# Kernel optimization log

Hardware: AMD Instinct MI355X
Metric: run time of the kernel (lower is better)

Reference implementation:

```python
import jax, jax.numpy as jnp
import numpy as np

B, L, D, DIN, S, R, K = 2, 1024, 1024, 2048, 16, 64, 4


def setup_inputs() -> dict:
    key = jax.random.key(0)
    ks = jax.random.split(key, 8)
    f = lambda k, sh, sc: jax.random.normal(k, sh, jnp.float32) * sc
    return {
        "x": f(ks[0], (B, L, D), 1.0),
        "norm_w": jnp.ones((D,), jnp.float32),
        "W_in": f(ks[1], (D, 2 * DIN), D ** -0.5),
        "conv_w": f(ks[2], (DIN, 1, K), 0.5),
        "conv_b": jnp.zeros((DIN,), jnp.float32),
        "W_x": f(ks[3], (DIN, R + 2 * S), DIN ** -0.5),
        "W_dt": f(ks[4], (R, DIN), R ** -0.5),
        "b_dt": f(ks[5], (DIN,), 0.1),
        "A_log": jnp.log(jnp.broadcast_to(jnp.arange(1, S + 1, dtype=jnp.float32), (DIN, S))),
        "D_skip": jnp.ones((DIN,), jnp.float32),
        "W_out": f(ks[6], (DIN, D), DIN ** -0.5),
    }


def reference(x, norm_w, W_in, conv_w, conv_b, W_x, W_dt, b_dt, A_log, D_skip, W_out):
    eps = 1e-5
    # RMSNorm
    xn = x * jax.lax.rsqrt(jnp.mean(x * x, axis=-1, keepdims=True) + eps) * norm_w
    # input projection -> (x_branch, gate)
    xz = xn @ W_in                       # [B,L,2*DIN]
    xi, z = jnp.split(xz, 2, axis=-1)
    # causal depthwise conv1d along L
    xt = jnp.transpose(xi, (0, 2, 1))    # [B,DIN,L]
    xc = jax.lax.conv_general_dilated(xt, conv_w, (1,), [(K - 1, 0)],
                                      feature_group_count=DIN)
    xc = jnp.transpose(xc, (0, 2, 1)) + conv_b
    xc = jax.nn.silu(xc)                 # [B,L,DIN]
    # input-dependent SSM parameters
    xd = xc @ W_x                        # [B,L,R+2S]
    dt, Bm, Cm = jnp.split(xd, [R, R + S], axis=-1)
    dt = jax.nn.softplus(dt @ W_dt + b_dt)           # [B,L,DIN]
    A = -jnp.exp(A_log)                              # [DIN,S]
    dA = jnp.exp(dt[..., None] * A)                  # [B,L,DIN,S]
    dBu = (dt * xc)[..., None] * Bm[:, :, None, :]   # [B,L,DIN,S]
    # selective scan: h_t = dA_t * h_{t-1} + dBu_t (parallel associative scan)
    def comb(c1, c2):
        a1, b1 = c1
        a2, b2 = c2
        return a1 * a2, a2 * b1 + b2
    _, h = jax.lax.associative_scan(comb, (dA, dBu), axis=1)
    y = jnp.einsum('blds,bls->bld', h, Cm) + D_skip * xc
    y = y * jax.nn.silu(z)
    return x + y @ W_out
```

## Files before the change

kernel.cpp:

```cpp
#include <hip/hip_runtime.h>

#define B_    2
#define L_    1024
#define D_    1024
#define DIN_  2048
#define S_    16
#define R_    64
#define NTOK  (B_ * L_)
#define NCH   32
#define LC    (L_ / NCH)

typedef unsigned short u16;
typedef short bf16x8 __attribute__((ext_vector_type(8)));
typedef float f32x4  __attribute__((ext_vector_type(4)));

__device__ __forceinline__ u16 f2bf(float f) {
    union { float f; unsigned u; } v; v.f = f;
    return (u16)((v.u + 0x7FFFu + ((v.u >> 16) & 1u)) >> 16);
}

__global__ __launch_bounds__(256) void rmsnorm_kernel(
    const float* __restrict__ x, const float* __restrict__ w, u16* __restrict__ xn) {
    int row = blockIdx.x;
    const float4 v = ((const float4*)(x + (size_t)row * D_))[threadIdx.x];
    float ss = v.x * v.x + v.y * v.y + v.z * v.z + v.w * v.w;
#pragma unroll
    for (int o = 32; o > 0; o >>= 1) ss += __shfl_down(ss, o);
    __shared__ float red[4];
    if ((threadIdx.x & 63) == 0) red[threadIdx.x >> 6] = ss;
    __syncthreads();
    float tot = red[0] + red[1] + red[2] + red[3];
    float sc = rsqrtf(tot * (1.f / (float)D_) + 1e-5f);
    const float4 wv = ((const float4*)w)[threadIdx.x];
    ushort4 o;
    o.x = f2bf(v.x * sc * wv.x);
    o.y = f2bf(v.y * sc * wv.y);
    o.z = f2bf(v.z * sc * wv.z);
    o.w = f2bf(v.w * sc * wv.w);
    ((ushort4*)(xn + (size_t)row * D_))[threadIdx.x] = o;
}

__global__ __launch_bounds__(256) void transpose_f32_to_bf16(
    const float* __restrict__ src, u16* __restrict__ dst, int R, int Csrc) {
    __shared__ float tile[32][33];
    int c0 = blockIdx.x * 32, r0 = blockIdx.y * 32;
    int tx = threadIdx.x & 31, ty = threadIdx.x >> 5;
#pragma unroll
    for (int i = 0; i < 32; i += 8)
        tile[ty + i][tx] = (c0 + tx < Csrc)
            ? src[(size_t)(r0 + ty + i) * Csrc + c0 + tx] : 0.f;
    __syncthreads();
#pragma unroll
    for (int i = 0; i < 32; i += 8)
        dst[(size_t)(c0 + ty + i) * R + r0 + tx] = f2bf(tile[tx][ty + i]);
}

#define BK 32
template<int BM, int BN>
__global__ __launch_bounds__(256) void gemm_bf16(
    const u16* __restrict__ A, int lda,
    const u16* __restrict__ Bt, int ldb,
    float* __restrict__ C, u16* __restrict__ Cbf, int ldc,
    const float* __restrict__ aux,
    int M, int N, int K, int mode) {
    constexpr int WGM = (BM >= 128) ? 2 : 1;
    constexpr int WGN = 4 / WGM;
    constexpr int FM = BM / (16 * WGM);
    constexpr int FN = BN / (16 * WGN);
    constexpr int ABYTES = BM * BK * 2;
    constexpr int BBYTES = BN * BK * 2;
    __shared__ __align__(16) u16 As[2][BM * BK];
    __shared__ __align__(16) u16 Bs[2][BN * BK];
    const int t = threadIdx.x;
    const int w = t >> 6;
    const int l = t & 63;
    const int lr = l & 15;
    const int kg = l >> 4;
    const int wm = (w / WGN) * (BM / WGM);
    const int wn = (w % WGN) * (BN / WGN);

    int nwg = gridDim.x * gridDim.y * gridDim.z;
    int flat = blockIdx.x + gridDim.x * (blockIdx.y + gridDim.y * blockIdx.z);
    int swz = (flat & 7) * (nwg >> 3) + (flat >> 3);
    int bx = swz % gridDim.x;
    int rem = swz / gridDim.x;
    int by = rem % gridDim.y;
    int bz = rem / gridDim.y;

    const int row0 = by * BM;
    const int col0 = bx * BN;
    const int kbase = bz * K;

    auto stage = [&](int buf, int k0) {
#pragma unroll
        for (int i = 0; i < ABYTES; i += 4096) {
            int off = i + t * 16;
            int grow = off >> 6;
            int sw = ((off >> 4) & 3) ^ ((grow >> 1) & 3);
            const u16* ga = A + (size_t)(row0 + grow) * lda + k0 + sw * 8;
            __builtin_amdgcn_global_load_lds(
                (const __attribute__((address_space(1))) unsigned int*)(const void*)ga,
                (__attribute__((address_space(3))) unsigned int*)(void*)&As[buf][off >> 1],
                16, 0, 0);
        }
#pragma unroll
        for (int i = 0; i < BBYTES; i += 4096) {
            int off = i + t * 16;
            int grow = off >> 6;
            int sw = ((off >> 4) & 3) ^ ((grow >> 1) & 3);
            const u16* gb = Bt + (size_t)(col0 + grow) * ldb + k0 + sw * 8;
            __builtin_amdgcn_global_load_lds(
                (const __attribute__((address_space(1))) unsigned int*)(const void*)gb,
                (__attribute__((address_space(3))) unsigned int*)(void*)&Bs[buf][off >> 1],
                16, 0, 0);
        }
    };

    f32x4 acc[FM][FN];
#pragma unroll
    for (int i = 0; i < FM; ++i)
#pragma unroll
        for (int j = 0; j < FN; ++j) acc[i][j] = (f32x4){0.f, 0.f, 0.f, 0.f};

    const int nt = K / BK;
    stage(0, kbase);
    asm volatile("s_waitcnt vmcnt(0)" ::: "memory");
    __builtin_amdgcn_s_barrier();
    asm volatile("" ::: "memory");

    int cur = 0;
    for (int tt = 0; tt < nt; ++tt) {
        if (tt + 1 < nt) stage(cur ^ 1, kbase + (tt + 1) * BK);
        bf16x8 af[FM], bfr[FN];
#pragma unroll
        for (int mt = 0; mt < FM; ++mt) {
            int ar = wm + mt * 16 + lr;
            af[mt] = *(const bf16x8*)&As[cur][ar * 32 + (kg ^ ((ar >> 1) & 3)) * 8];
        }
#pragma unroll
        for (int nt2 = 0; nt2 < FN; ++nt2) {
            int br = wn + nt2 * 16 + lr;
            bfr[nt2] = *(const bf16x8*)&Bs[cur][br * 32 + (kg ^ ((br >> 1) & 3)) * 8];
        }
        __builtin_amdgcn_s_setprio(1);
#pragma unroll
        for (int mt = 0; mt < FM; ++mt)
#pragma unroll
            for (int nt2 = 0; nt2 < FN; ++nt2)
                acc[mt][nt2] = __builtin_amdgcn_mfma_f32_16x16x32_bf16(
                    af[mt], bfr[nt2], acc[mt][nt2], 0, 0, 0);
        __builtin_amdgcn_s_setprio(0);
        if (tt + 1 < nt) {
            asm volatile("s_waitcnt vmcnt(0)" ::: "memory");
            __builtin_amdgcn_s_barrier();
            asm volatile("" ::: "memory");
        }
        cur ^= 1;
    }

    size_t pbase = (mode == 3) ? (size_t)bz * M * N : 0;
#pragma unroll
    for (int mt = 0; mt < FM; ++mt) {
#pragma unroll
        for (int nt2 = 0; nt2 < FN; ++nt2) {
#pragma unroll
            for (int r = 0; r < 4; ++r) {
                int row = row0 + wm + mt * 16 + kg * 4 + r;
                int col = col0 + wn + nt2 * 16 + lr;
                float v = acc[mt][nt2][r];
                if (mode == 1) { v += aux[col]; v = (v > 20.f) ? v : log1pf(__expf(v)); }
                else if (mode == 2) { v += aux[(size_t)row * ldc + col]; }
                if (C)   C[pbase + (size_t)row * ldc + col] = v;
                if (Cbf) Cbf[(size_t)row * ldc + col] = f2bf(v);
            }
        }
    }
}

__global__ __launch_bounds__(256) void reduce_wx_kernel(
    const float* __restrict__ part, float* __restrict__ xd, u16* __restrict__ xdb) {
    int i = blockIdx.x * 256 + threadIdx.x;
    float4 s = ((const float4*)part)[i];
#pragma unroll
    for (int k = 1; k < 16; ++k) {
        float4 v = ((const float4*)(part + (size_t)k * NTOK * 128))[i];
        s.x += v.x; s.y += v.y; s.z += v.z; s.w += v.w;
    }
    ((float4*)xd)[i] = s;
    ushort4 o; o.x = f2bf(s.x); o.y = f2bf(s.y); o.z = f2bf(s.z); o.w = f2bf(s.w);
    ((ushort4*)xdb)[i] = o;
}

__global__ __launch_bounds__(256) void reduce_out_kernel(
    const float* __restrict__ part, const float* __restrict__ x, float* __restrict__ out) {
    int i = blockIdx.x * 256 + threadIdx.x;
    float4 s = ((const float4*)part)[i];
#pragma unroll
    for (int k = 1; k < 4; ++k) {
        float4 v = ((const float4*)(part + (size_t)k * NTOK * D_))[i];
        s.x += v.x; s.y += v.y; s.z += v.z; s.w += v.w;
    }
    float4 xv = ((const float4*)x)[i];
    s.x += xv.x; s.y += xv.y; s.z += xv.z; s.w += xv.w;
    ((float4*)out)[i] = s;
}

__global__ __launch_bounds__(256) void conv_silu_kernel(
    const float* __restrict__ xz, const float* __restrict__ cw,
    const float* __restrict__ cb, float* __restrict__ xc, u16* __restrict__ xcb) {
    size_t idx = (size_t)blockIdx.x * 256 + threadIdx.x;
    int c = (int)(idx & (DIN_ - 1));
    int bl = (int)(idx >> 11);
    int l = bl & (L_ - 1);
    const float4 w = ((const float4*)cw)[c];
    float s0 = (l >= 3) ? xz[(size_t)(bl - 3) * 4096 + c] : 0.f;
    float s1 = (l >= 2) ? xz[(size_t)(bl - 2) * 4096 + c] : 0.f;
    float s2 = (l >= 1) ? xz[(size_t)(bl - 1) * 4096 + c] : 0.f;
    float s3 = xz[(size_t)bl * 4096 + c];
    float acc = cb[c] + s0 * w.x + s1 * w.y + s2 * w.z + s3 * w.w;
    float v = acc / (1.f + __expf(-acc));
    xc[idx] = v;
    xcb[idx] = f2bf(v);
}

__global__ __launch_bounds__(256) void scan_chunk_kernel(
    const float* __restrict__ dt, const float* __restrict__ xc,
    const float* __restrict__ xd, const float* __restrict__ A_log,
    float* __restrict__ Pout, float* __restrict__ Hout) {
    int din = blockIdx.x * 256 + threadIdx.x;
    int c = blockIdx.y, b = blockIdx.z;
    float a[S_], h[S_];
#pragma unroll
    for (int q = 0; q < 4; ++q) {
        float4 av = ((const float4*)(A_log + (size_t)din * S_))[q];
        a[q * 4 + 0] = -__expf(av.x); a[q * 4 + 1] = -__expf(av.y);
        a[q * 4 + 2] = -__expf(av.z); a[q * 4 + 3] = -__expf(av.w);
    }
#pragma unroll
    for (int s = 0; s < S_; ++s) h[s] = 0.f;
    float sdt = 0.f;
    size_t rbase = (size_t)b * L_ + (size_t)c * LC;
#pragma unroll 2
    for (int i = 0; i < LC; ++i) {
        size_t row = rbase + i;
        float dtv = dt[row * DIN_ + din];
        float xcv = xc[row * DIN_ + din];
        float du = dtv * xcv;
        sdt += dtv;
        const float4* bp = (const float4*)(xd + row * 128 + 64);
        float4 B0 = bp[0], B1 = bp[1], B2 = bp[2], B3 = bp[3];
        float Bv[S_] = {B0.x, B0.y, B0.z, B0.w, B1.x, B1.y, B1.z, B1.w,
                        B2.x, B2.y, B2.z, B2.w, B3.x, B3.y, B3.z, B3.w};
#pragma unroll
        for (int s = 0; s < S_; ++s) {
            float dA = __expf(dtv * a[s]);
            h[s] = h[s] * dA + du * Bv[s];
        }
    }
    size_t obase = ((size_t)(b * NCH + c) * DIN_ + din) * S_;
#pragma unroll
    for (int q = 0; q < 4; ++q) {
        float4 pv, hv;
        pv.x = __expf(a[q * 4 + 0] * sdt); pv.y = __expf(a[q * 4 + 1] * sdt);
        pv.z = __expf(a[q * 4 + 2] * sdt); pv.w = __expf(a[q * 4 + 3] * sdt);
        hv.x = h[q * 4 + 0]; hv.y = h[q * 4 + 1]; hv.z = h[q * 4 + 2]; hv.w = h[q * 4 + 3];
        ((float4*)(Pout + obase))[q] = pv;
        ((float4*)(Hout + obase))[q] = hv;
    }
}

__global__ __launch_bounds__(256) void scan_combine_kernel(
    const float* __restrict__ P, const float* __restrict__ H,
    float* __restrict__ h0) {
    int tid = blockIdx.x * 256 + threadIdx.x;
    int ds = tid & (DIN_ * S_ - 1);
    int b = tid >> 15;
    float h = 0.f;
#pragma unroll
    for (int c = 0; c < NCH; ++c) {
        size_t idx = ((size_t)(b * NCH + c) * DIN_ * S_) + ds;
        h0[idx] = h;
        h = H[idx] + P[idx] * h;
    }
}

__global__ __launch_bounds__(256) void scan_final_kernel(
    const float* __restrict__ dt, const float* __restrict__ xc,
    const float* __restrict__ xd, const float* __restrict__ A_log,
    const float* __restrict__ h0, const float* __restrict__ Dskip,
    const float* __restrict__ xz, u16* __restrict__ yg) {
    int din = blockIdx.x * 256 + threadIdx.x;
    int c = blockIdx.y, b = blockIdx.z;
    float a[S_], h[S_];
#pragma unroll
    for (int q = 0; q < 4; ++q) {
        float4 av = ((const float4*)(A_log + (size_t)din * S_))[q];
        a[q * 4 + 0] = -__expf(av.x); a[q * 4 + 1] = -__expf(av.y);
        a[q * 4 + 2] = -__expf(av.z); a[q * 4 + 3] = -__expf(av.w);
    }
    size_t ibase = ((size_t)(b * NCH + c) * DIN_ + din) * S_;
#pragma unroll
    for (int q = 0; q < 4; ++q) {
        float4 hv = ((const float4*)(h0 + ibase))[q];
        h[q * 4 + 0] = hv.x; h[q * 4 + 1] = hv.y; h[q * 4 + 2] = hv.z; h[q * 4 + 3] = hv.w;
    }
    float dsk = Dskip[din];
    size_t rbase = (size_t)b * L_ + (size_t)c * LC;
#pragma unroll 2
    for (int i = 0; i < LC; ++i) {
        size_t row = rbase + i;
        float dtv = dt[row * DIN_ + din];
        float xcv = xc[row * DIN_ + din];
        float du = dtv * xcv;
        const float4* bp = (const float4*)(xd + row * 128 + 64);
        float4 B0 = bp[0], B1 = bp[1], B2 = bp[2], B3 = bp[3];
        const float4* cp = (const float4*)(xd + row * 128 + 80);
        float4 C0 = cp[0], C1 = cp[1], C2 = cp[2], C3 = cp[3];
        float Bv[S_] = {B0.x, B0.y, B0.z, B0.w, B1.x, B1.y, B1.z, B1.w,
                        B2.x, B2.y, B2.z, B2.w, B3.x, B3.y, B3.z, B3.w};
        float Cv[S_] = {C0.x, C0.y, C0.z, C0.w, C1.x, C1.y, C1.z, C1.w,
                        C2.x, C2.y, C2.z, C2.w, C3.x, C3.y, C3.z, C3.w};
        float py = 0.f;
#pragma unroll
        for (int s = 0; s < S_; ++s) {
            float dA = __expf(dtv * a[s]);
            h[s] = h[s] * dA + du * Bv[s];
            py += h[s] * Cv[s];
        }
        float zv = xz[row * 4096 + DIN_ + din];
        float y = (py + dsk * xcv) * (zv / (1.f + __expf(-zv)));
        yg[row * DIN_ + din] = f2bf(y);
    }
}

extern "C" void kernel_launch(void* const* d_in, const int* in_sizes, int n_in,
                              void* d_out, int out_size, void* d_ws, size_t ws_size,
                              hipStream_t stream) {
    const float* x      = (const float*)d_in[0];
    const float* norm_w = (const float*)d_in[1];
    const float* W_in   = (const float*)d_in[2];
    const float* conv_w = (const float*)d_in[3];
    const float* conv_b = (const float*)d_in[4];
    const float* W_x    = (const float*)d_in[5];
    const float* W_dt   = (const float*)d_in[6];
    const float* b_dt   = (const float*)d_in[7];
    const float* A_log  = (const float*)d_in[8];
    const float* D_skip = (const float*)d_in[9];
    const float* W_out  = (const float*)d_in[10];
    float* out = (float*)d_out;

    char* p = (char*)d_ws;
    auto alloc = [&](size_t bytes) {
        char* r = p;
        p += (bytes + 255) & ~(size_t)255;
        return r;
    };
    u16*   xn    = (u16*)alloc((size_t)NTOK * D_ * 2);
    u16*   WinT  = (u16*)alloc((size_t)2 * DIN_ * D_ * 2);
    u16*   WoutT = (u16*)alloc((size_t)D_ * DIN_ * 2);
    u16*   WxT   = (u16*)alloc((size_t)128 * DIN_ * 2);
    u16*   WdtT  = (u16*)alloc((size_t)DIN_ * R_ * 2);
    float* xz    = (float*)alloc((size_t)NTOK * 2 * DIN_ * 4);
    float* xc    = (float*)alloc((size_t)NTOK * DIN_ * 4);
    u16*   xcb   = (u16*)alloc((size_t)NTOK * DIN_ * 2);
    float* xd    = (float*)alloc((size_t)NTOK * 128 * 4);
    u16*   xdb   = (u16*)alloc((size_t)NTOK * 128 * 2);
    float* dtb   = (float*)alloc((size_t)NTOK * DIN_ * 4);
    u16*   yg    = (u16*)alloc((size_t)NTOK * DIN_ * 2);
    float* Pbuf  = (float*)alloc((size_t)B_ * NCH * DIN_ * S_ * 4);
    float* Hbuf  = (float*)alloc((size_t)B_ * NCH * DIN_ * S_ * 4);
    float* h0buf = (float*)alloc((size_t)B_ * NCH * DIN_ * S_ * 4);

    float* part_wx  = dtb;
    float* part_out = xz;

    rmsnorm_kernel<<<NTOK, 256, 0, stream>>>(x, norm_w, xn);
    transpose_f32_to_bf16<<<dim3(2 * DIN_ / 32, D_ / 32), 256, 0, stream>>>(W_in, WinT, D_, 2 * DIN_);
    transpose_f32_to_bf16<<<dim3(D_ / 32, DIN_ / 32), 256, 0, stream>>>(W_out, WoutT, DIN_, D_);
    transpose_f32_to_bf16<<<dim3(128 / 32, DIN_ / 32), 256, 0, stream>>>(W_x, WxT, DIN_, 96);
    transpose_f32_to_bf16<<<dim3(DIN_ / 32, R_ / 32), 256, 0, stream>>>(W_dt, WdtT, R_, DIN_);

    gemm_bf16<64, 128><<<dim3(2 * DIN_ / 128, NTOK / 64), 256, 0, stream>>>(
        xn, D_, WinT, D_, xz, nullptr, 2 * DIN_, nullptr, NTOK, 2 * DIN_, D_, 0);
    conv_silu_kernel<<<(NTOK * DIN_) / 256, 256, 0, stream>>>(xz, conv_w, conv_b, xc, xcb);
    gemm_bf16<64, 128><<<dim3(1, NTOK / 64, 16), 256, 0, stream>>>(
        xcb, DIN_, WxT, DIN_, part_wx, nullptr, 128, nullptr, NTOK, 128, DIN_ / 16, 3);
    reduce_wx_kernel<<<(NTOK * 128 / 4) / 256, 256, 0, stream>>>(part_wx, xd, xdb);
    gemm_bf16<64, 128><<<dim3(DIN_ / 128, NTOK / 64), 256, 0, stream>>>(
        xdb, 128, WdtT, R_, dtb, nullptr, DIN_, b_dt, NTOK, DIN_, R_, 1);
    {
        dim3 grid(DIN_ / 256, NCH, B_);
        scan_chunk_kernel<<<grid, 256, 0, stream>>>(dtb, xc, xd, A_log, Pbuf, Hbuf);
        scan_combine_kernel<<<(B_ * DIN_ * S_) / 256, 256, 0, stream>>>(Pbuf, Hbuf, h0buf);
        scan_final_kernel<<<grid, 256, 0, stream>>>(dtb, xc, xd, A_log, h0buf, D_skip, xz, yg);
    }
    gemm_bf16<64, 128><<<dim3(D_ / 128, NTOK / 64, 4), 256, 0, stream>>>(
        yg, DIN_, WoutT, DIN_, part_out, nullptr, D_, nullptr, NTOK, D_, DIN_ / 4, 3);
    reduce_out_kernel<<<(NTOK * D_ / 4) / 256, 256, 0, stream>>>(part_out, x, out);
}
```

Baseline: 184.2 us.

## Merge weight transposes, deepen GEMM K-tile, drop fp32 conv buffer

Fuses the four weight-transpose launches into one kernel that dispatches tiles by block index. Raises the GEMM K-tile from 32 to 64, with a new 8-way XOR LDS swizzle and two MFMA sub-steps per stage, which halves the barrier and stage count. The conv kernel now computes four time steps per thread from a shared 7-element window and writes only the bf16 output. The scan kernels read that bf16 copy instead of an fp32 one, saving memory traffic at a small cost in precision in the scan inputs. The larger K-tile doubles LDS use, which may lower occupancy.

Result: no change. 187.0 us (+1.5%).

```diff
diff --git a/kernel.cpp b/kernel.cpp
--- a/kernel.cpp
+++ b/kernel.cpp
@@ -17,6 +17,10 @@
 __device__ __forceinline__ u16 f2bf(float f) {
     union { float f; unsigned u; } v; v.f = f;
     return (u16)((v.u + 0x7FFFu + ((v.u >> 16) & 1u)) >> 16);
+}
+__device__ __forceinline__ float bf2f(u16 b) {
+    union { unsigned u; float f; } v; v.u = (unsigned)b << 16;
+    return v.f;
 }
 
 __global__ __launch_bounds__(256) void rmsnorm_kernel(
@@ -40,11 +44,11 @@
     ((ushort4*)(xn + (size_t)row * D_))[threadIdx.x] = o;
 }
 
-__global__ __launch_bounds__(256) void transpose_f32_to_bf16(
-    const float* __restrict__ src, u16* __restrict__ dst, int R, int Csrc) {
+__device__ __forceinline__ void transp_tile(
+    const float* __restrict__ src, u16* __restrict__ dst,
+    int R, int Csrc, int cx, int cy, int tx, int ty) {
     __shared__ float tile[32][33];
-    int c0 = blockIdx.x * 32, r0 = blockIdx.y * 32;
-    int tx = threadIdx.x & 31, ty = threadIdx.x >> 5;
+    int c0 = cx * 32, r0 = cy * 32;
 #pragma unroll
     for (int i = 0; i < 32; i += 8)
         tile[ty + i][tx] = (c0 + tx < Csrc)
@@ -55,7 +59,28 @@
         dst[(size_t)(c0 + ty + i) * R + r0 + tx] = f2bf(tile[tx][ty + i]);
 }
 
-#define BK 32
+__global__ __launch_bounds__(256) void transpose_all_kernel(
+    const float* __restrict__ W_in,  u16* __restrict__ WinT,
+    const float* __restrict__ W_out, u16* __restrict__ WoutT,
+    const float* __restrict__ W_x,   u16* __restrict__ WxT,
+    const float* __restrict__ W_dt,  u16* __restrict__ WdtT) {
+    int bid = blockIdx.x;
+    int tx = threadIdx.x & 31, ty = threadIdx.x >> 5;
+    if (bid < 4096) {
+        transp_tile(W_in, WinT, D_, 2 * DIN_, bid % 128, bid / 128, tx, ty);
+    } else if (bid < 6144) {
+        int b = bid - 4096;
+        transp_tile(W_out, WoutT, DIN_, D_, b % 32, b / 32, tx, ty);
+    } else if (bid < 6400) {
+        int b = bid - 6144;
+        transp_tile(W_x, WxT, DIN_, 96, b % 4, b / 4, tx, ty);
+    } else {
+        int b = bid - 6400;
+        transp_tile(W_dt, WdtT, R_, DIN_, b % 64, b / 64, tx, ty);
+    }
+}
+
+#define BK 64
 template<int BM, int BN>
 __global__ __launch_bounds__(256) void gemm_bf16(
     const u16* __restrict__ A, int lda,
@@ -95,8 +120,8 @@
 #pragma unroll
         for (int i = 0; i < ABYTES; i += 4096) {
             int off = i + t * 16;
-            int grow = off >> 6;
-            int sw = ((off >> 4) & 3) ^ ((grow >> 1) & 3);
+            int grow = off >> 7;
+            int sw = ((off >> 4) & 7) ^ (grow & 7);
             const u16* ga = A + (size_t)(row0 + grow) * lda + k0 + sw * 8;
             __builtin_amdgcn_global_load_lds(
                 (const __attribute__((address_space(1))) unsigned int*)(const void*)ga,
@@ -106,8 +131,8 @@
 #pragma unroll
         for (int i = 0; i < BBYTES; i += 4096) {
             int off = i + t * 16;
-            int grow = off >> 6;
-            int sw = ((off >> 4) & 3) ^ ((grow >> 1) & 3);
+            int grow = off >> 7;
+            int sw = ((off >> 4) & 7) ^ (grow & 7);
             const u16* gb = Bt + (size_t)(col0 + grow) * ldb + k0 + sw * 8;
             __builtin_amdgcn_global_load_lds(
                 (const __attribute__((address_space(1))) unsigned int*)(const void*)gb,
@@ -131,25 +156,28 @@
     int cur = 0;
     for (int tt = 0; tt < nt; ++tt) {
         if (tt + 1 < nt) stage(cur ^ 1, kbase + (tt + 1) * BK);
-        bf16x8 af[FM], bfr[FN];
-#pragma unroll
-        for (int mt = 0; mt < FM; ++mt) {
-            int ar = wm + mt * 16 + lr;
-            af[mt] = *(const bf16x8*)&As[cur][ar * 32 + (kg ^ ((ar >> 1) & 3)) * 8];
-        }
-#pragma unroll
-        for (int nt2 = 0; nt2 < FN; ++nt2) {
-            int br = wn + nt2 * 16 + lr;
-            bfr[nt2] = *(const bf16x8*)&Bs[cur][br * 32 + (kg ^ ((br >> 1) & 3)) * 8];
-        }
-        __builtin_amdgcn_s_setprio(1);
-#pragma unroll
-        for (int mt = 0; mt < FM; ++mt)
-#pragma unroll
-            for (int nt2 = 0; nt2 < FN; ++nt2)
-                acc[mt][nt2] = __builtin_amdgcn_mfma_f32_16x16x32_bf16(
-                    af[mt], bfr[nt2], acc[mt][nt2], 0, 0, 0);
-        __builtin_amdgcn_s_setprio(0);
+#pragma unroll
+        for (int ks = 0; ks < 2; ++ks) {
+            bf16x8 af[FM], bfr[FN];
+#pragma unroll
+            for (int mt = 0; mt < FM; ++mt) {
+                int ar = wm + mt * 16 + lr;
+                af[mt] = *(const bf16x8*)&As[cur][ar * 64 + (((ks << 2) | kg) ^ (ar & 7)) * 8];
+            }
+#pragma unroll
+            for (int nt2 = 0; nt2 < FN; ++nt2) {
+                int br = wn + nt2 * 16 + lr;
+                bfr[nt2] = *(const bf16x8*)&Bs[cur][br * 64 + (((ks << 2) | kg) ^ (br & 7)) * 8];
+            }
+            __builtin_amdgcn_s_setprio(1);
+#pragma unroll
+            for (int mt = 0; mt < FM; ++mt)
+#pragma unroll
+                for (int nt2 = 0; nt2 < FN; ++nt2)
+                    acc[mt][nt2] = __builtin_amdgcn_mfma_f32_16x16x32_bf16(
+                        af[mt], bfr[nt2], acc[mt][nt2], 0, 0, 0);
+            __builtin_amdgcn_s_setprio(0);
+        }
         if (tt + 1 < nt) {
             asm volatile("s_waitcnt vmcnt(0)" ::: "memory");
             __builtin_amdgcn_s_barrier();
@@ -207,24 +235,30 @@
 
 __global__ __launch_bounds__(256) void conv_silu_kernel(
     const float* __restrict__ xz, const float* __restrict__ cw,
-    const float* __restrict__ cb, float* __restrict__ xc, u16* __restrict__ xcb) {
+    const float* __restrict__ cb, u16* __restrict__ xcb) {
     size_t idx = (size_t)blockIdx.x * 256 + threadIdx.x;
     int c = (int)(idx & (DIN_ - 1));
-    int bl = (int)(idx >> 11);
-    int l = bl & (L_ - 1);
+    int g = (int)(idx >> 11);
+    int bl0 = g * 4;
+    int l0 = bl0 & (L_ - 1);
     const float4 w = ((const float4*)cw)[c];
-    float s0 = (l >= 3) ? xz[(size_t)(bl - 3) * 4096 + c] : 0.f;
-    float s1 = (l >= 2) ? xz[(size_t)(bl - 2) * 4096 + c] : 0.f;
-    float s2 = (l >= 1) ? xz[(size_t)(bl - 1) * 4096 + c] : 0.f;
-    float s3 = xz[(size_t)bl * 4096 + c];
-    float acc = cb[c] + s0 * w.x + s1 * w.y + s2 * w.z + s3 * w.w;
-    float v = acc / (1.f + __expf(-acc));
-    xc[idx] = v;
-    xcb[idx] = f2bf(v);
+    float bias = cb[c];
+    float v[7];
+#pragma unroll
+    for (int k = 0; k < 7; ++k) {
+        int off = k - 3;
+        v[k] = (l0 + off >= 0) ? xz[(size_t)(bl0 + off) * 4096 + c] : 0.f;
+    }
+#pragma unroll
+    for (int j = 0; j < 4; ++j) {
+        float acc = bias + v[j] * w.x + v[j + 1] * w.y + v[j + 2] * w.z + v[j + 3] * w.w;
+        float s = acc / (1.f + __expf(-acc));
+        xcb[(size_t)(bl0 + j) * DIN_ + c] = f2bf(s);
+    }
 }
 
 __global__ __launch_bounds__(256) void scan_chunk_kernel(
-    const float* __restrict__ dt, const float* __restrict__ xc,
+    const float* __restrict__ dt, const u16* __restrict__ xcb,
     const float* __restrict__ xd, const float* __restrict__ A_log,
     float* __restrict__ Pout, float* __restrict__ Hout) {
     int din = blockIdx.x * 256 + threadIdx.x;
@@ -244,7 +278,7 @@
     for (int i = 0; i < LC; ++i) {
         size_t row = rbase + i;
         float dtv = dt[row * DIN_ + din];
-        float xcv = xc[row * DIN_ + din];
+        float xcv = bf2f(xcb[row * DIN_ + din]);
         float du = dtv * xcv;
         sdt += dtv;
         const float4* bp = (const float4*)(xd + row * 128 + 64);
@@ -285,7 +319,7 @@
 }
 
 __global__ __launch_bounds__(256) void scan_final_kernel(
-    const float* __restrict__ dt, const float* __restrict__ xc,
+    const float* __restrict__ dt, const u16* __restrict__ xcb,
     const float* __restrict__ xd, const float* __restrict__ A_log,
     const float* __restrict__ h0, const float* __restrict__ Dskip,
     const float* __restrict__ xz, u16* __restrict__ yg) {
@@ -310,7 +344,7 @@
     for (int i = 0; i < LC; ++i) {
         size_t row = rbase + i;
         float dtv = dt[row * DIN_ + din];
-        float xcv = xc[row * DIN_ + din];
+        float xcv = bf2f(xcb[row * DIN_ + din]);
         float du = dtv * xcv;
         const float4* bp = (const float4*)(xd + row * 128 + 64);
         float4 B0 = bp[0], B1 = bp[1], B2 = bp[2], B3 = bp[3];
@@ -361,7 +395,6 @@
     u16*   WxT   = (u16*)alloc((size_t)128 * DIN_ * 2);
     u16*   WdtT  = (u16*)alloc((size_t)DIN_ * R_ * 2);
     float* xz    = (float*)alloc((size_t)NTOK * 2 * DIN_ * 4);
-    float* xc    = (float*)alloc((size_t)NTOK * DIN_ * 4);
     u16*   xcb   = (u16*)alloc((size_t)NTOK * DIN_ * 2);
     float* xd    = (float*)alloc((size_t)NTOK * 128 * 4);
     u16*   xdb   = (u16*)alloc((size_t)NTOK * 128 * 2);
@@ -375,14 +408,12 @@
     float* part_out = xz;
 
     rmsnorm_kernel<<<NTOK, 256, 0, stream>>>(x, norm_w, xn);
-    transpose_f32_to_bf16<<<dim3(2 * DIN_ / 32, D_ / 32), 256, 0, stream>>>(W_in, WinT, D_, 2 * DIN_);
-    transpose_f32_to_bf16<<<dim3(D_ / 32, DIN_ / 32), 256, 0, stream>>>(W_out, WoutT, DIN_, D_);
-    transpose_f32_to_bf16<<<dim3(128 / 32, DIN_ / 32), 256, 0, stream>>>(W_x, WxT, DIN_, 96);
-    transpose_f32_to_bf16<<<dim3(DIN_ / 32, R_ / 32), 256, 0, stream>>>(W_dt, WdtT, R_, DIN_);
+    transpose_all_kernel<<<6528, 256, 0, stream>>>(
+        W_in, WinT, W_out, WoutT, W_x, WxT, W_dt, WdtT);
 
     gemm_bf16<64, 128><<<dim3(2 * DIN_ / 128, NTOK / 64), 256, 0, stream>>>(
         xn, D_, WinT, D_, xz, nullptr, 2 * DIN_, nullptr, NTOK, 2 * DIN_, D_, 0);
-    conv_silu_kernel<<<(NTOK * DIN_) / 256, 256, 0, stream>>>(xz, conv_w, conv_b, xc, xcb);
+    conv_silu_kernel<<<(NTOK * DIN_ / 4) / 256, 256, 0, stream>>>(xz, conv_w, conv_b, xcb);
     gemm_bf16<64, 128><<<dim3(1, NTOK / 64, 16), 256, 0, stream>>>(
         xcb, DIN_, WxT, DIN_, part_wx, nullptr, 128, nullptr, NTOK, 128, DIN_ / 16, 3);
     reduce_wx_kernel<<<(NTOK * 128 / 4) / 256, 256, 0, stream>>>(part_wx, xd, xdb);
@@ -390,9 +421,9 @@
         xdb, 128, WdtT, R_, dtb, nullptr, DIN_, b_dt, NTOK, DIN_, R_, 1);
     {
         dim3 grid(DIN_ / 256, NCH, B_);
-        scan_chunk_kernel<<<grid, 256, 0, stream>>>(dtb, xc, xd, A_log, Pbuf, Hbuf);
+        scan_chunk_kernel<<<grid, 256, 0, stream>>>(dtb, xcb, xd, A_log, Pbuf, Hbuf);
         scan_combine_kernel<<<(B_ * DIN_ * S_) / 256, 256, 0, stream>>>(Pbuf, Hbuf, h0buf);
-        scan_final_kernel<<<grid, 256, 0, stream>>>(dtb, xc, xd, A_log, h0buf, D_skip, xz, yg);
+        scan_final_kernel<<<grid, 256, 0, stream>>>(dtb, xcb, xd, A_log, h0buf, D_skip, xz, yg);
     }
     gemm_bf16<64, 128><<<dim3(D_ / 128, NTOK / 64, 4), 256, 0, stream>>>(
         yg, DIN_, WoutT, DIN_, part_out, nullptr, D_, nullptr, NTOK, D_, DIN_ / 4, 3);
```
